# Kernel tuning notes

Measured on AMD Instinct MI355X. Metric: run time of the kernel, lower is better.

## Reference

```python
import jax, jax.numpy as jnp
import numpy as np
from jax import lax


def _conv1x1(x, w, b=None):
    # x: [B,C,H,W], w: [O,C]
    y = jnp.einsum('bchw,oc->bohw', x, w)
    if b is not None:
        y = y + b[None, :, None, None]
    return y


def _lgce(x, pre_w, pre_b, w1, b1, w2, b2, sw, sb, post_w, post_b):
    # Local Group Context Enhancer on [B,64,H,W], 8 groups of 8 channels.
    b, c, h, wd = x.shape
    g = 8
    cg = c // g
    res = x
    x = _conv1x1(x, pre_w, pre_b)
    xg = x.reshape(b, g, cg, h, wd)
    # CBAM per group (vectorized over groups)
    pooled = xg.mean(axis=(3, 4))                                  # [b,g,cg]
    hid = jax.nn.relu(jnp.einsum('bgc,ghc->bgh', pooled, w1) + b1[None])
    cw = jax.nn.sigmoid(jnp.einsum('bgh,gch->bgc', hid, w2) + b2[None])
    xc = xg * cw[:, :, :, None, None]                              # channel gate
    sp = jax.nn.sigmoid(jnp.einsum('bgchw,goc->bgohw', xc, sw) + sb[None, :, :, None, None])
    cbam_out = xc * sp                                             # spatial gate
    resp = jax.nn.sigmoid(cbam_out)
    thr = resp.mean(axis=(2, 3, 4), keepdims=True)                 # per (batch, group)
    mask = jnp.where(resp > thr, jnp.ones_like(resp), resp)
    x = (xg * mask).reshape(b, c, h, wd)
    x = _conv1x1(x, post_w, post_b)
    return x + res


def setup_inputs() -> dict:
    key = jax.random.key(0)
    ks = jax.random.split(key, 20)
    f = lambda k, s: (jax.random.normal(k, s) * 0.02).astype(jnp.float32)
    return {
        'x': jax.random.normal(ks[0], (4, 128, 256, 256), dtype=jnp.float32),
        'input_proj_w': f(ks[1], (128, 128)),
        'lgce_pre_w': f(ks[2], (64, 64)), 'lgce_pre_b': f(ks[3], (64,)),
        'cbam_w1': f(ks[4], (8, 2, 8)), 'cbam_b1': f(ks[5], (8, 2)),
        'cbam_w2': f(ks[6], (8, 8, 2)), 'cbam_b2': f(ks[7], (8, 8)),
        'cbam_sw': f(ks[8], (8, 1, 8)), 'cbam_sb': f(ks[9], (8, 1)),
        'lgce_post_w': f(ks[10], (64, 64)), 'lgce_post_b': f(ks[11], (64,)),
        'qkv_w': f(ks[12], (192, 64)),
        'dw_w': f(ks[13], (192, 1, 3, 3)),
        'gate_w1': f(ks[14], (32, 64)), 'gate_b1': f(ks[15], (32,)),
        'gate_w2': f(ks[16], (1, 32)), 'gate_b2': f(ks[17], (1,)),
        'temperature': jnp.ones((8, 1, 1), jnp.float32),
        'scales': jnp.full((4,), 0.2, jnp.float32),
        'proj_out_w': f(ks[18], (128, 128)),
    }


def reference(x, input_proj_w, lgce_pre_w, lgce_pre_b, cbam_w1, cbam_b1,
              cbam_w2, cbam_b2, cbam_sw, cbam_sb, lgce_post_w, lgce_post_b,
              qkv_w, dw_w, gate_w1, gate_b1, gate_w2, gate_b2,
              temperature, scales, proj_out_w):
    b, c, h, wd = x.shape
    heads = 8
    proj = _conv1x1(x, input_proj_w)
    lb, gb = jnp.split(proj, 2, axis=1)                            # local / global
    lb = _lgce(lb, lgce_pre_w, lgce_pre_b, cbam_w1, cbam_b1, cbam_w2, cbam_b2,
               cbam_sw, cbam_sb, lgce_post_w, lgce_post_b)
    qkv = _conv1x1(gb, qkv_w)
    qkv = lax.conv_general_dilated(qkv, dw_w, (1, 1), 'SAME',
                                   feature_group_count=192,
                                   dimension_numbers=('NCHW', 'OIHW', 'NCHW'))
    q, k, v = jnp.split(qkv, 3, axis=1)
    hw = h * wd
    cph = (c // 2) // heads                                        # channels per head
    to_heads = lambda t: t.reshape(b, heads, cph, hw)
    q, k, v = to_heads(q), to_heads(k), to_heads(v)
    q = q / jnp.maximum(jnp.linalg.norm(q, axis=-1, keepdims=True), 1e-12)
    k = k / jnp.maximum(jnp.linalg.norm(k, axis=-1, keepdims=True), 1e-12)
    attn = jnp.einsum('bhcn,bhdn->bhcd', q, k) * temperature[None]  # [b,h,cph,cph]
    # dynamic top-k from global gate (single scalar over whole batch, as original)
    gate = jax.nn.sigmoid(_conv1x1(jax.nn.relu(_conv1x1(gb, gate_w1, gate_b1)),
                                   gate_w2, gate_b2))
    kdyn = jnp.clip(jnp.floor(cph * gate.mean()), 1.0, float(cph))
    # rank-based top-k mask (jit-safe equivalent of topk+scatter)
    ranks = jnp.argsort(jnp.argsort(-attn, axis=-1), axis=-1)
    attn = jnp.where(ranks < kdyn, attn, -jnp.inf)
    attn = jax.nn.softmax(attn, axis=-1)
    out = jnp.einsum('bhcd,bhdn->bhcn', attn, v) * scales.sum()
    out = out.reshape(b, c // 2, h, wd)
    fused = jnp.concatenate([out, lb], axis=1)
    return _conv1x1(fused, proj_out_w)
```

## Files before the change

### kernel.cpp

```cpp
#include <hip/hip_runtime.h>
#include <math.h>

#define HWN 65536

__device__ __forceinline__ float sgm(float x){ return 1.0f/(1.0f+expf(-x)); }

__device__ __forceinline__ void fma4(float acc[4], const float4 w,
                                     const float4 x0, const float4 x1,
                                     const float4 x2, const float4 x3){
    acc[0] += w.x*x0.x + w.y*x1.x + w.z*x2.x + w.w*x3.x;
    acc[1] += w.x*x0.y + w.y*x1.y + w.z*x2.y + w.w*x3.y;
    acc[2] += w.x*x0.z + w.y*x1.z + w.z*x2.z + w.w*x3.z;
    acc[3] += w.x*x0.w + w.y*x1.w + w.z*x2.w + w.w*x3.w;
}

__global__ __launch_bounds__(256,2) void k1_proj(
    const float* __restrict__ x,   const float* __restrict__ Wp,
    const float* __restrict__ Wpre,const float* __restrict__ bpre,
    const float* __restrict__ Wqkv,
    const float* __restrict__ Wg1, const float* __restrict__ bg1,
    const float* __restrict__ wg2, const float* __restrict__ bg2,
    float* __restrict__ lb, float* __restrict__ pre, float* __restrict__ qkv,
    float* __restrict__ pooled_part, float* __restrict__ gate_part)
{
    __shared__ float st[128*128];
    float4* st4 = (float4*)st;
    float*  ht  = st;

    const int t    = threadIdx.x;
    const int blk  = blockIdx.x;
    const int b    = blk >> 9;
    const int p0   = (blk & 511) << 7;
    const int pg   = t & 15;
    const int og   = t >> 4;
    const int slot = blk & 63;

    const float4* x4 = (const float4*)x;

    #pragma unroll
    for (int i = 0; i < 16; ++i) {
        int idx = t + 256*i;
        int c = idx >> 5, q = idx & 31;
        st4[c*32 + q] = x4[(size_t)(b*128 + c)*16384 + (p0>>2) + q];
    }
    __syncthreads();

    {
        const int o0 = og*8;
        float acc[8][8];
        #pragma unroll
        for (int j=0;j<8;++j)
            #pragma unroll
            for (int k=0;k<8;++k) acc[j][k]=0.f;
        const float4* W4 = (const float4*)Wp;
        #pragma unroll 2
        for (int c = 0; c < 128; c += 4) {
            float4 xa0 = st4[(c+0)*32 + pg],      xb0 = st4[(c+0)*32 + 16 + pg];
            float4 xa1 = st4[(c+1)*32 + pg],      xb1 = st4[(c+1)*32 + 16 + pg];
            float4 xa2 = st4[(c+2)*32 + pg],      xb2 = st4[(c+2)*32 + 16 + pg];
            float4 xa3 = st4[(c+3)*32 + pg],      xb3 = st4[(c+3)*32 + 16 + pg];
            #pragma unroll
            for (int j = 0; j < 8; ++j) {
                float4 w = W4[(o0+j)*32 + (c>>2)];
                fma4(&acc[j][0], w, xa0,xa1,xa2,xa3);
                fma4(&acc[j][4], w, xb0,xb1,xb2,xb3);
            }
        }
        __syncthreads();

        #pragma unroll
        for (int j = 0; j < 8; ++j) {
            st4[(o0+j)*32 + pg]      = make_float4(acc[j][0],acc[j][1],acc[j][2],acc[j][3]);
            st4[(o0+j)*32 + 16 + pg] = make_float4(acc[j][4],acc[j][5],acc[j][6],acc[j][7]);
        }
        if (og < 8) {
            float4* lb4 = (float4*)lb;
            #pragma unroll
            for (int j = 0; j < 8; ++j) {
                lb4[(size_t)(b*64 + o0+j)*16384 + (p0>>2) + pg] =
                    make_float4(acc[j][0],acc[j][1],acc[j][2],acc[j][3]);
                lb4[(size_t)(b*64 + o0+j)*16384 + (p0>>2) + 16 + pg] =
                    make_float4(acc[j][4],acc[j][5],acc[j][6],acc[j][7]);
            }
        }
    }
    __syncthreads();

    {
        const int o0 = og*4;
        float acc[4][8];
        #pragma unroll
        for (int j=0;j<4;++j)
            #pragma unroll
            for (int k=0;k<8;++k) acc[j][k]=0.f;
        const float4* W4 = (const float4*)Wpre;
        #pragma unroll 2
        for (int c = 0; c < 64; c += 4) {
            float4 xa0 = st4[(c+0)*32 + pg],      xb0 = st4[(c+0)*32 + 16 + pg];
            float4 xa1 = st4[(c+1)*32 + pg],      xb1 = st4[(c+1)*32 + 16 + pg];
            float4 xa2 = st4[(c+2)*32 + pg],      xb2 = st4[(c+2)*32 + 16 + pg];
            float4 xa3 = st4[(c+3)*32 + pg],      xb3 = st4[(c+3)*32 + 16 + pg];
            #pragma unroll
            for (int j = 0; j < 4; ++j) {
                float4 w = W4[(o0+j)*16 + (c>>2)];
                fma4(&acc[j][0], w, xa0,xa1,xa2,xa3);
                fma4(&acc[j][4], w, xb0,xb1,xb2,xb3);
            }
        }
        float4* pre4 = (float4*)pre;
        #pragma unroll
        for (int j = 0; j < 4; ++j) {
            float bs = bpre[o0+j];
            float4 v0 = make_float4(acc[j][0]+bs, acc[j][1]+bs, acc[j][2]+bs, acc[j][3]+bs);
            float4 v1 = make_float4(acc[j][4]+bs, acc[j][5]+bs, acc[j][6]+bs, acc[j][7]+bs);
            pre4[(size_t)(b*64 + o0+j)*16384 + (p0>>2) + pg]      = v0;
            pre4[(size_t)(b*64 + o0+j)*16384 + (p0>>2) + 16 + pg] = v1;
            float s = v0.x+v0.y+v0.z+v0.w + v1.x+v1.y+v1.z+v1.w;
            s += __shfl_xor(s,1); s += __shfl_xor(s,2);
            s += __shfl_xor(s,4); s += __shfl_xor(s,8);
            if (pg == 0) atomicAdd(&pooled_part[slot*256 + b*64 + o0 + j], s);
        }
    }

    #pragma unroll
    for (int chk = 0; chk < 2; ++chk) {
        const int o0 = og*12 + chk*6;
        float acc[6][8];
        #pragma unroll
        for (int j=0;j<6;++j)
            #pragma unroll
            for (int k=0;k<8;++k) acc[j][k]=0.f;
        const float4* W4 = (const float4*)Wqkv;
        #pragma unroll 2
        for (int c = 0; c < 64; c += 4) {
            float4 xa0 = st4[(64+c+0)*32 + pg],   xb0 = st4[(64+c+0)*32 + 16 + pg];
            float4 xa1 = st4[(64+c+1)*32 + pg],   xb1 = st4[(64+c+1)*32 + 16 + pg];
            float4 xa2 = st4[(64+c+2)*32 + pg],   xb2 = st4[(64+c+2)*32 + 16 + pg];
            float4 xa3 = st4[(64+c+3)*32 + pg],   xb3 = st4[(64+c+3)*32 + 16 + pg];
            #pragma unroll
            for (int j = 0; j < 6; ++j) {
                float4 w = W4[(o0+j)*16 + (c>>2)];
                fma4(&acc[j][0], w, xa0,xa1,xa2,xa3);
                fma4(&acc[j][4], w, xb0,xb1,xb2,xb3);
            }
        }
        float4* qkv4 = (float4*)qkv;
        #pragma unroll
        for (int j = 0; j < 6; ++j) {
            qkv4[(size_t)(b*192 + o0+j)*16384 + (p0>>2) + pg] =
                make_float4(acc[j][0],acc[j][1],acc[j][2],acc[j][3]);
            qkv4[(size_t)(b*192 + o0+j)*16384 + (p0>>2) + 16 + pg] =
                make_float4(acc[j][4],acc[j][5],acc[j][6],acc[j][7]);
        }
    }

    {
        const int o0 = og*2;
        float acc[2][8];
        #pragma unroll
        for (int j=0;j<2;++j)
            #pragma unroll
            for (int k=0;k<8;++k) acc[j][k]=0.f;
        const float4* W4 = (const float4*)Wg1;
        for (int c = 0; c < 64; c += 4) {
            float4 xa0 = st4[(64+c+0)*32 + pg],   xb0 = st4[(64+c+0)*32 + 16 + pg];
            float4 xa1 = st4[(64+c+1)*32 + pg],   xb1 = st4[(64+c+1)*32 + 16 + pg];
            float4 xa2 = st4[(64+c+2)*32 + pg],   xb2 = st4[(64+c+2)*32 + 16 + pg];
            float4 xa3 = st4[(64+c+3)*32 + pg],   xb3 = st4[(64+c+3)*32 + 16 + pg];
            #pragma unroll
            for (int j = 0; j < 2; ++j) {
                float4 w = W4[(o0+j)*16 + (c>>2)];
                fma4(&acc[j][0], w, xa0,xa1,xa2,xa3);
                fma4(&acc[j][4], w, xb0,xb1,xb2,xb3);
            }
        }
        __syncthreads();
        #pragma unroll
        for (int j = 0; j < 2; ++j) {
            float bs = bg1[o0+j];
            #pragma unroll
            for (int k = 0; k < 4; ++k) {
                ht[(o0+j)*128 + pg*4 + k]      = fmaxf(acc[j][k]+bs,   0.0f);
                ht[(o0+j)*128 + 64 + pg*4 + k] = fmaxf(acc[j][4+k]+bs, 0.0f);
            }
        }
    }
    __syncthreads();

    if (t < 128) {
        float g = bg2[0];
        #pragma unroll
        for (int c = 0; c < 32; ++c) g += wg2[c]*ht[c*128 + t];
        g = sgm(g);
        g += __shfl_xor(g,1);  g += __shfl_xor(g,2);  g += __shfl_xor(g,4);
        g += __shfl_xor(g,8);  g += __shfl_xor(g,16); g += __shfl_xor(g,32);
        if ((t & 63) == 0) atomicAdd(&gate_part[slot], g);
    }
}

__global__ void k2_small(const float* __restrict__ pooled_part,
                         const float* __restrict__ gate_part,
                         const float* __restrict__ w1, const float* __restrict__ b1,
                         const float* __restrict__ w2, const float* __restrict__ b2,
                         float* __restrict__ cw, float* __restrict__ kdyn)
{
    __shared__ float pl[256];
    const int t = threadIdx.x;
    float s = 0.f;
    for (int sl = 0; sl < 64; ++sl) s += pooled_part[sl*256 + t];
    pl[t] = s * (1.0f/65536.0f);
    __syncthreads();
    const int b = t >> 6, g = (t >> 3) & 7, c = t & 7;
    float h0 = b1[g*2+0], h1 = b1[g*2+1];
    #pragma unroll
    for (int cc = 0; cc < 8; ++cc) {
        float p = pl[b*64 + g*8 + cc];
        h0 += p*w1[g*16 + 0*8 + cc];
        h1 += p*w1[g*16 + 1*8 + cc];
    }
    h0 = fmaxf(h0, 0.f); h1 = fmaxf(h1, 0.f);
    cw[t] = sgm(h0*w2[g*16 + c*2 + 0] + h1*w2[g*16 + c*2 + 1] + b2[g*8+c]);
    if (t == 0) {
        float gs = 0.f;
        for (int sl = 0; sl < 64; ++sl) gs += gate_part[sl];
        float kd = floorf(8.0f * (gs * (1.0f/262144.0f)));
        *kdyn = fminf(fmaxf(kd, 1.0f), 8.0f);
    }
}

#define K4_ROWSTRIDE 264
#define K4_BUF (10*K4_ROWSTRIDE)

__global__ __launch_bounds__(256,3) void k4_dw(
    const float* __restrict__ qkv, const float* __restrict__ dww,
    const float* __restrict__ pre, const float* __restrict__ cw,
    const float* __restrict__ sw,  const float* __restrict__ sb,
    float* __restrict__ v, float* __restrict__ Sg, float* __restrict__ sumsq,
    float* __restrict__ thr_sum)
{
    __shared__ float sh[2*K4_BUF];

    const int t    = threadIdx.x;
    const int b    = blockIdx.x >> 8;
    const int h    = (blockIdx.x >> 5) & 7;
    const int band = blockIdx.x & 31;
    const int r0   = band * 8;
    const int lr   = t >> 5;
    const int c0   = (t & 31) * 4;
    const int lane = t & 63;

    if (t < 40) {
        int bufi = t / 20, r = (t % 20) >> 1, side = t & 1;
        sh[bufi*K4_BUF + r*K4_ROWSTRIDE + (side ? 260 : 3)] = 0.0f;
    }

    float4 reg[3];

    auto issue_loads = [&](int ch) {
        const float4* base = (const float4*)(qkv + (size_t)(b*192 + ch)*HWN);
        #pragma unroll
        for (int j = 0; j < 3; ++j) {
            int i = t + 256*j;
            float4 val = make_float4(0.f,0.f,0.f,0.f);
            if (i < 640) {
                int row = i >> 6, col4 = i & 63;
                int gy = r0 - 1 + row;
                if (gy >= 0 && gy < 256) val = base[gy*64 + col4];
            }
            reg[j] = val;
        }
    };

    auto write_lds = [&](float* buf) {
        #pragma unroll
        for (int j = 0; j < 3; ++j) {
            int i = t + 256*j;
            if (i < 640) {
                int row = i >> 6, col4 = i & 63;
                *(float4*)&buf[row*K4_ROWSTRIDE + 4 + col4*4] = reg[j];
            }
        }
    };

    auto conv8 = [&](const float* buf, const float* __restrict__ w9, float out[8]) {
        #pragma unroll
        for (int g = 0; g < 2; ++g) {
            const int cc = c0 + g*128;
            float a0=0.f, a1=0.f, a2=0.f, a3=0.f;
            #pragma unroll
            for (int rr = 0; rr < 3; ++rr) {
                const float* row = &buf[(lr+rr)*K4_ROWSTRIDE + 4 + cc];
                float4 m = *(const float4*)row;
                float l = row[-1], r = row[4];
                float w0 = w9[rr*3+0], w1 = w9[rr*3+1], w2 = w9[rr*3+2];
                a0 = fmaf(w0,l,   fmaf(w1,m.x, fmaf(w2,m.y, a0)));
                a1 = fmaf(w0,m.x, fmaf(w1,m.y, fmaf(w2,m.z, a1)));
                a2 = fmaf(w0,m.y, fmaf(w1,m.z, fmaf(w2,m.w, a2)));
                a3 = fmaf(w0,m.z, fmaf(w1,m.w, fmaf(w2,r,   a3)));
            }
            out[g*4+0]=a0; out[g*4+1]=a1; out[g*4+2]=a2; out[g*4+3]=a3;
        }
    };

    auto wsum = [&](float val) {
        val += __shfl_xor(val,1);  val += __shfl_xor(val,2);  val += __shfl_xor(val,4);
        val += __shfl_xor(val,8);  val += __shfl_xor(val,16); val += __shfl_xor(val,32);
        return val;
    };

    float dq[8][8];

    float* sq_q = &sumsq[b*128 + h*8];
    float* sq_k = &sumsq[b*128 + 64 + h*8];
    float* Sgb  = &Sg[(size_t)(b*8+h)*64];

    issue_loads(h*8 + 0);

    #pragma unroll
    for (int ch = 0; ch < 8; ++ch) {
        float* buf = sh + (ch & 1)*K4_BUF;
        write_lds(buf);
        issue_loads(ch < 7 ? (h*8 + ch + 1) : (64 + h*8));
        __syncthreads();
        conv8(buf, dww + (h*8 + ch)*9, dq[ch]);
        float ss = 0.f;
        #pragma unroll
        for (int p = 0; p < 8; ++p) ss = fmaf(dq[ch][p], dq[ch][p], ss);
        ss = wsum(ss);
        if (lane == 0) atomicAdd(&sq_q[ch], ss);
    }

    #pragma unroll
    for (int ch = 0; ch < 8; ++ch) {
        float* buf = sh + (ch & 1)*K4_BUF;
        write_lds(buf);
        issue_loads(ch < 7 ? (64 + h*8 + ch + 1) : (128 + h*8));
        __syncthreads();
        float dk[8];
        conv8(buf, dww + (64 + h*8 + ch)*9, dk);
        float ss = 0.f;
        #pragma unroll
        for (int p = 0; p < 8; ++p) ss = fmaf(dk[p], dk[p], ss);
        ss = wsum(ss);
        if (lane == 0) atomicAdd(&sq_k[ch], ss);
        #pragma unroll
        for (int c = 0; c < 8; ++c) {
            float acc = 0.f;
            #pragma unroll
            for (int p = 0; p < 8; ++p) acc = fmaf(dq[c][p], dk[p], acc);
            acc = wsum(acc);
            if (lane == 0) atomicAdd(&Sgb[c*8 + ch], acc);
        }
    }

    #pragma unroll
    for (int ch = 0; ch < 8; ++ch) {
        float* buf = sh + (ch & 1)*K4_BUF;
        write_lds(buf);
        if (ch < 7) issue_loads(128 + h*8 + ch + 1);
        __syncthreads();
        float dv[8];
        conv8(buf, dww + (128 + h*8 + ch)*9, dv);
        float* vb = v + (size_t)(b*64 + h*8 + ch)*HWN + (r0 + lr)*256;
        *(float4*)&vb[c0]       = make_float4(dv[0],dv[1],dv[2],dv[3]);
        *(float4*)&vb[c0 + 128] = make_float4(dv[4],dv[5],dv[6],dv[7]);
    }

    {
        float cwr[8], swr[8];
        #pragma unroll
        for (int c = 0; c < 8; ++c) {
            cwr[c] = cw[b*64 + h*8 + c];
            swr[c] = sw[h*8 + c];
        }
        const float sbg = sb[h];
        float rs = 0.f;
        const float* preb = pre + (size_t)(b*64 + h*8)*HWN + (size_t)(r0 + lr)*256;
        #pragma unroll
        for (int g2 = 0; g2 < 2; ++g2) {
            const int cc = c0 + g2*128;
            float xc[8][4];
            float spa0 = sbg, spa1 = sbg, spa2 = sbg, spa3 = sbg;
            #pragma unroll
            for (int c = 0; c < 8; ++c) {
                float4 xv = *(const float4*)&preb[(size_t)c*HWN + cc];
                xc[c][0] = xv.x*cwr[c]; xc[c][1] = xv.y*cwr[c];
                xc[c][2] = xv.z*cwr[c]; xc[c][3] = xv.w*cwr[c];
                spa0 = fmaf(xc[c][0], swr[c], spa0);
                spa1 = fmaf(xc[c][1], swr[c], spa1);
                spa2 = fmaf(xc[c][2], swr[c], spa2);
                spa3 = fmaf(xc[c][3], swr[c], spa3);
            }
            float sp0 = sgm(spa0), sp1 = sgm(spa1), sp2 = sgm(spa2), sp3 = sgm(spa3);
            #pragma unroll
            for (int c = 0; c < 8; ++c) {
                rs += sgm(xc[c][0]*sp0);
                rs += sgm(xc[c][1]*sp1);
                rs += sgm(xc[c][2]*sp2);
                rs += sgm(xc[c][3]*sp3);
            }
        }
        rs = wsum(rs);
        if (lane == 0) atomicAdd(&thr_sum[b*8 + h], rs);
    }
}

__global__ void k6_attn(const float* __restrict__ Sg, const float* __restrict__ sumsq,
                        const float* __restrict__ temp, const float* __restrict__ kdynp,
                        const float* __restrict__ thr_sum, const float* __restrict__ scales,
                        float* __restrict__ A, float* __restrict__ thr)
{
    const int t = threadIdx.x;
    if (t < 32) thr[t] = thr_sum[t] * (1.0f/(8.0f*65536.0f));
    const int b = t >> 6, h = (t >> 3) & 7, c = t & 7;
    const float kd = *kdynp;
    const float ssum = scales[0]+scales[1]+scales[2]+scales[3];
    const float nq = fmaxf(sqrtf(sumsq[b*128 + h*8 + c]), 1e-12f);
    const float tv = temp[h];
    const float* Srow = Sg + (size_t)(b*8+h)*64 + c*8;
    float a[8];
    #pragma unroll
    for (int d = 0; d < 8; ++d) {
        float nk = fmaxf(sqrtf(sumsq[b*128 + 64 + h*8 + d]), 1e-12f);
        a[d] = Srow[d] / (nq*nk) * tv;
    }
    bool keep[8];
    #pragma unroll
    for (int d = 0; d < 8; ++d) {
        int r = 0;
        #pragma unroll
        for (int e = 0; e < 8; ++e)
            r += (a[e] > a[d]) || (a[e] == a[d] && e < d);
        keep[d] = ((float)r < kd);
    }
    float m = -INFINITY;
    #pragma unroll
    for (int d = 0; d < 8; ++d) if (keep[d]) m = fmaxf(m, a[d]);
    float ex[8]; float sum = 0.f;
    #pragma unroll
    for (int d = 0; d < 8; ++d) { ex[d] = keep[d] ? expf(a[d]-m) : 0.f; sum += ex[d]; }
    const float inv = ssum / sum;
    #pragma unroll
    for (int d = 0; d < 8; ++d)
        A[(size_t)(b*8+h)*64 + c*8 + d] = ex[d]*inv;
}

__global__ __launch_bounds__(256,2) void k7_final(
    const float* __restrict__ pre, const float* __restrict__ lb, const float* __restrict__ v,
    const float* __restrict__ cw,  const float* __restrict__ thr,
    const float* __restrict__ sw,  const float* __restrict__ sb,
    const float* __restrict__ A,
    const float* __restrict__ Wpost, const float* __restrict__ bpost,
    const float* __restrict__ Wout,  float* __restrict__ out)
{
    __shared__ float pr[64*128];
    __shared__ float vt[64*128];
    float4* pr4 = (float4*)pr;
    float4* vt4 = (float4*)vt;

    const int t   = threadIdx.x;
    const int blk = blockIdx.x;
    const int b   = blk >> 9;
    const int p0  = (blk & 511) << 7;
    const int pg  = t & 15;
    const int og  = t >> 4;

    const float4* pre4g = (const float4*)pre;
    const float4* v4g   = (const float4*)v;
    #pragma unroll
    for (int i = 0; i < 8; ++i) {
        int idx = t + 256*i;
        int c = idx >> 5, q = idx & 31;
        size_t gi = (size_t)(b*64 + c)*16384 + (p0>>2) + q;
        pr4[c*32+q] = pre4g[gi];
        vt4[c*32+q] = v4g[gi];
    }
    __syncthreads();

    #pragma unroll
    for (int s = 0; s < 4; ++s) {
        int task = t + 256*s;
        int g = task >> 7, px = task & 127;
        float xc[8], xv[8];
        float spa = sb[g];
        #pragma unroll
        for (int c = 0; c < 8; ++c) {
            xv[c] = pr[(g*8+c)*128 + px];
            xc[c] = xv[c]*cw[b*64 + g*8 + c];
            spa += xc[c]*sw[g*8 + c];
        }
        float sp = sgm(spa);
        float th = thr[b*8 + g];
        #pragma unroll
        for (int c = 0; c < 8; ++c) {
            float resp = sgm(xc[c]*sp);
            float mask = resp > th ? 1.0f : resp;
            pr[(g*8+c)*128 + px] = xv[c]*mask;
        }
    }
    __syncthreads();

    float postv[4][8];
    {
        const int o0 = og*4;
        float acc[4][8];
        #pragma unroll
        for (int j=0;j<4;++j)
            #pragma unroll
            for (int k=0;k<8;++k) acc[j][k]=0.f;
        const float4* W4 = (const float4*)Wpost;
        #pragma unroll 2
        for (int c = 0; c < 64; c += 4) {
            float4 xa0 = pr4[(c+0)*32 + pg],      xb0 = pr4[(c+0)*32 + 16 + pg];
            float4 xa1 = pr4[(c+1)*32 + pg],      xb1 = pr4[(c+1)*32 + 16 + pg];
            float4 xa2 = pr4[(c+2)*32 + pg],      xb2 = pr4[(c+2)*32 + 16 + pg];
            float4 xa3 = pr4[(c+3)*32 + pg],      xb3 = pr4[(c+3)*32 + 16 + pg];
            #pragma unroll
            for (int j = 0; j < 4; ++j) {
                float4 w = W4[(o0+j)*16 + (c>>2)];
                fma4(&acc[j][0], w, xa0,xa1,xa2,xa3);
                fma4(&acc[j][4], w, xb0,xb1,xb2,xb3);
            }
        }
        const float4* lb4 = (const float4*)lb;
        #pragma unroll
        for (int j = 0; j < 4; ++j) {
            float bs = bpost[o0+j];
            float4 l0 = lb4[(size_t)(b*64 + o0+j)*16384 + (p0>>2) + pg];
            float4 l1 = lb4[(size_t)(b*64 + o0+j)*16384 + (p0>>2) + 16 + pg];
            postv[j][0]=acc[j][0]+bs+l0.x; postv[j][1]=acc[j][1]+bs+l0.y;
            postv[j][2]=acc[j][2]+bs+l0.z; postv[j][3]=acc[j][3]+bs+l0.w;
            postv[j][4]=acc[j][4]+bs+l1.x; postv[j][5]=acc[j][5]+bs+l1.y;
            postv[j][6]=acc[j][6]+bs+l1.z; postv[j][7]=acc[j][7]+bs+l1.w;
        }
    }

    float attv[4][8];
    {
        const int ch0 = og*4;
        #pragma unroll
        for (int j = 0; j < 4; ++j) {
            int ch = ch0 + j;
            int hh = ch >> 3, c = ch & 7;
            const float* Ar = A + (size_t)(b*8+hh)*64 + c*8;
            float a0=0.f,a1=0.f,a2=0.f,a3=0.f,a4=0.f,a5=0.f,a6=0.f,a7=0.f;
            #pragma unroll
            for (int d = 0; d < 8; ++d) {
                float av = Ar[d];
                float4 v0 = vt4[(hh*8+d)*32 + pg];
                float4 v1 = vt4[(hh*8+d)*32 + 16 + pg];
                a0 += av*v0.x; a1 += av*v0.y; a2 += av*v0.z; a3 += av*v0.w;
                a4 += av*v1.x; a5 += av*v1.y; a6 += av*v1.z; a7 += av*v1.w;
            }
            attv[j][0]=a0; attv[j][1]=a1; attv[j][2]=a2; attv[j][3]=a3;
            attv[j][4]=a4; attv[j][5]=a5; attv[j][6]=a6; attv[j][7]=a7;
        }
    }
    __syncthreads();

    {
        const int o0 = og*4;
        #pragma unroll
        for (int j = 0; j < 4; ++j) {
            vt4[(o0+j)*32 + pg]      = make_float4(attv[j][0],attv[j][1],attv[j][2],attv[j][3]);
            vt4[(o0+j)*32 + 16 + pg] = make_float4(attv[j][4],attv[j][5],attv[j][6],attv[j][7]);
            pr4[(o0+j)*32 + pg]      = make_float4(postv[j][0],postv[j][1],postv[j][2],postv[j][3]);
            pr4[(o0+j)*32 + 16 + pg] = make_float4(postv[j][4],postv[j][5],postv[j][6],postv[j][7]);
        }
    }
    __syncthreads();

    {
        const int o0 = og*8;
        float acc[8][8];
        #pragma unroll
        for (int j=0;j<8;++j)
            #pragma unroll
            for (int k=0;k<8;++k) acc[j][k]=0.f;
        const float4* W4 = (const float4*)Wout;
        #pragma unroll 2
        for (int c = 0; c < 64; c += 4) {
            float4 xa0 = vt4[(c+0)*32 + pg],      xb0 = vt4[(c+0)*32 + 16 + pg];
            float4 xa1 = vt4[(c+1)*32 + pg],      xb1 = vt4[(c+1)*32 + 16 + pg];
            float4 xa2 = vt4[(c+2)*32 + pg],      xb2 = vt4[(c+2)*32 + 16 + pg];
            float4 xa3 = vt4[(c+3)*32 + pg],      xb3 = vt4[(c+3)*32 + 16 + pg];
            #pragma unroll
            for (int j = 0; j < 8; ++j) {
                float4 w = W4[(o0+j)*32 + (c>>2)];
                fma4(&acc[j][0], w, xa0,xa1,xa2,xa3);
                fma4(&acc[j][4], w, xb0,xb1,xb2,xb3);
            }
        }
        #pragma unroll 2
        for (int c = 0; c < 64; c += 4) {
            float4 xa0 = pr4[(c+0)*32 + pg],      xb0 = pr4[(c+0)*32 + 16 + pg];
            float4 xa1 = pr4[(c+1)*32 + pg],      xb1 = pr4[(c+1)*32 + 16 + pg];
            float4 xa2 = pr4[(c+2)*32 + pg],      xb2 = pr4[(c+2)*32 + 16 + pg];
            float4 xa3 = pr4[(c+3)*32 + pg],      xb3 = pr4[(c+3)*32 + 16 + pg];
            #pragma unroll
            for (int j = 0; j < 8; ++j) {
                float4 w = W4[(o0+j)*32 + 16 + (c>>2)];
                fma4(&acc[j][0], w, xa0,xa1,xa2,xa3);
                fma4(&acc[j][4], w, xb0,xb1,xb2,xb3);
            }
        }
        float4* out4 = (float4*)out;
        #pragma unroll
        for (int j = 0; j < 8; ++j) {
            out4[(size_t)(b*128 + o0+j)*16384 + (p0>>2) + pg] =
                make_float4(acc[j][0],acc[j][1],acc[j][2],acc[j][3]);
            out4[(size_t)(b*128 + o0+j)*16384 + (p0>>2) + 16 + pg] =
                make_float4(acc[j][4],acc[j][5],acc[j][6],acc[j][7]);
        }
    }
}

extern "C" void kernel_launch(void* const* d_in, const int* in_sizes, int n_in,
                              void* d_out, int out_size, void* d_ws, size_t ws_size,
                              hipStream_t stream)
{
    const float* x     = (const float*)d_in[0];
    const float* Wp    = (const float*)d_in[1];
    const float* Wpre  = (const float*)d_in[2];
    const float* bpre  = (const float*)d_in[3];
    const float* w1    = (const float*)d_in[4];
    const float* b1    = (const float*)d_in[5];
    const float* w2    = (const float*)d_in[6];
    const float* b2    = (const float*)d_in[7];
    const float* sw    = (const float*)d_in[8];
    const float* sb    = (const float*)d_in[9];
    const float* Wpost = (const float*)d_in[10];
    const float* bpost = (const float*)d_in[11];
    const float* Wqkv  = (const float*)d_in[12];
    const float* dww   = (const float*)d_in[13];
    const float* Wg1   = (const float*)d_in[14];
    const float* bg1   = (const float*)d_in[15];
    const float* wg2   = (const float*)d_in[16];
    const float* bg2   = (const float*)d_in[17];
    const float* temp  = (const float*)d_in[18];
    const float* scales= (const float*)d_in[19];
    const float* Wout  = (const float*)d_in[20];
    float* out = (float*)d_out;

    float* ws = (float*)d_ws;
    float* pooled_part = ws;
    float* gate_part   = ws + 16384;
    float* thr_sum     = ws + 16448;
    float* sumsq       = ws + 16480;
    float* Sg          = ws + 16992;
    float* cw          = ws + 19040;
    float* kdyn        = ws + 19296;
    float* thr         = ws + 19328;
    float* A           = ws + 19360;

    float* lb  = ws + 32768;
    float* pre = lb  + 16777216;
    float* qkv = pre + 16777216;
    float* v   = qkv + 50331648;

    hipMemsetAsync(ws, 0, (size_t)19040*sizeof(float), stream);

    k1_proj <<<2048, 256, 0, stream>>>(x, Wp, Wpre, bpre, Wqkv, Wg1, bg1, wg2, bg2,
                                       lb, pre, qkv, pooled_part, gate_part);
    k2_small<<<1,    256, 0, stream>>>(pooled_part, gate_part, w1, b1, w2, b2, cw, kdyn);
    k4_dw   <<<1024, 256, 0, stream>>>(qkv, dww, pre, cw, sw, sb, v, Sg, sumsq, thr_sum);
    k6_attn <<<1,    256, 0, stream>>>(Sg, sumsq, temp, kdyn, thr_sum, scales, A, thr);
    k7_final<<<2048, 256, 0, stream>>>(pre, lb, v, cw, thr, sw, sb, A,
                                       Wpost, bpost, Wout, out);
}
```

Baseline: 797.0 us.

## Use split-bf16 MFMA for final output projection in k7_final

Replaces the scalar FP32 FMA loop of the final 128->128 output projection with bf16 MFMA instructions. Each FP32 operand is split into hi and lo bf16 parts and three MFMAs are issued per tile to keep accuracy close to FP32. Activations are repacked into a transposed, XOR-swizzled bf16 layout in shared memory. The trade-off is extra packing work, scalar (non-vectorized) output stores, and a small precision loss from dropping the lo*lo term.

```diff
diff --git a/kernel.cpp b/kernel.cpp
--- a/kernel.cpp
+++ b/kernel.cpp
@@ -3,7 +3,14 @@
 
 #define HWN 65536
 
+typedef __attribute__((ext_vector_type(8))) short bf16x8;
+typedef __attribute__((ext_vector_type(4))) float f32x4;
+
 __device__ __forceinline__ float sgm(float x){ return 1.0f/(1.0f+expf(-x)); }
+
+__device__ __forceinline__ unsigned pack_hi2(float a, float b){
+    return (__float_as_uint(b) & 0xFFFF0000u) | (__float_as_uint(a) >> 16);
+}
 
 __device__ __forceinline__ void fma4(float acc[4], const float4 w,
                                      const float4 x0, const float4 x1,
@@ -453,10 +460,15 @@
     const float* __restrict__ Wpost, const float* __restrict__ bpost,
     const float* __restrict__ Wout,  float* __restrict__ out)
 {
-    __shared__ float pr[64*128];
-    __shared__ float vt[64*128];
+    __shared__ float smem[16384];
+    float* pr = smem;
+    float* vt = smem + 8192;
     float4* pr4 = (float4*)pr;
     float4* vt4 = (float4*)vt;
+    unsigned* XThi32 = (unsigned*)smem;
+    unsigned* XTlo32 = (unsigned*)(smem + 8192);
+    const unsigned short* XThi = (const unsigned short*)smem;
+    const unsigned short* XTlo = (const unsigned short*)(smem + 8192);
 
     const int t   = threadIdx.x;
     const int blk = blockIdx.x;
@@ -559,58 +571,79 @@
     __syncthreads();
 
     {
-        const int o0 = og*4;
-        #pragma unroll
-        for (int j = 0; j < 4; ++j) {
-            vt4[(o0+j)*32 + pg]      = make_float4(attv[j][0],attv[j][1],attv[j][2],attv[j][3]);
-            vt4[(o0+j)*32 + 16 + pg] = make_float4(attv[j][4],attv[j][5],attv[j][6],attv[j][7]);
-            pr4[(o0+j)*32 + pg]      = make_float4(postv[j][0],postv[j][1],postv[j][2],postv[j][3]);
-            pr4[(o0+j)*32 + 16 + pg] = make_float4(postv[j][4],postv[j][5],postv[j][6],postv[j][7]);
+        #pragma unroll
+        for (int half = 0; half < 2; ++half) {
+            #pragma unroll
+            for (int k = 0; k < 4; ++k) {
+                const int px = half*64 + pg*4 + k;
+                const int sw2 = (px & 7) << 2;
+                const int rowb = px*64;
+                #pragma unroll
+                for (int jj = 0; jj < 4; jj += 2) {
+                    float a0 = attv[jj][half*4+k], a1 = attv[jj+1][half*4+k];
+                    int i32 = (rowb + ((og*4+jj)>>1)) ^ sw2;
+                    XThi32[i32] = pack_hi2(a0, a1);
+                    float ah0 = __uint_as_float(__float_as_uint(a0)&0xFFFF0000u);
+                    float ah1 = __uint_as_float(__float_as_uint(a1)&0xFFFF0000u);
+                    XTlo32[i32] = pack_hi2(a0-ah0, a1-ah1);
+                    float q0 = postv[jj][half*4+k], q1 = postv[jj+1][half*4+k];
+                    i32 = (rowb + ((64+og*4+jj)>>1)) ^ sw2;
+                    XThi32[i32] = pack_hi2(q0, q1);
+                    float qh0 = __uint_as_float(__float_as_uint(q0)&0xFFFF0000u);
+                    float qh1 = __uint_as_float(__float_as_uint(q1)&0xFFFF0000u);
+                    XTlo32[i32] = pack_hi2(q0-qh0, q1-qh1);
+                }
+            }
         }
     }
     __syncthreads();
 
     {
-        const int o0 = og*8;
-        float acc[8][8];
-        #pragma unroll
-        for (int j=0;j<8;++j)
-            #pragma unroll
-            for (int k=0;k<8;++k) acc[j][k]=0.f;
-        const float4* W4 = (const float4*)Wout;
-        #pragma unroll 2
-        for (int c = 0; c < 64; c += 4) {
-            float4 xa0 = vt4[(c+0)*32 + pg],      xb0 = vt4[(c+0)*32 + 16 + pg];
-            float4 xa1 = vt4[(c+1)*32 + pg],      xb1 = vt4[(c+1)*32 + 16 + pg];
-            float4 xa2 = vt4[(c+2)*32 + pg],      xb2 = vt4[(c+2)*32 + 16 + pg];
-            float4 xa3 = vt4[(c+3)*32 + pg],      xb3 = vt4[(c+3)*32 + 16 + pg];
-            #pragma unroll
-            for (int j = 0; j < 8; ++j) {
-                float4 w = W4[(o0+j)*32 + (c>>2)];
-                fma4(&acc[j][0], w, xa0,xa1,xa2,xa3);
-                fma4(&acc[j][4], w, xb0,xb1,xb2,xb3);
-            }
-        }
-        #pragma unroll 2
-        for (int c = 0; c < 64; c += 4) {
-            float4 xa0 = pr4[(c+0)*32 + pg],      xb0 = pr4[(c+0)*32 + 16 + pg];
-            float4 xa1 = pr4[(c+1)*32 + pg],      xb1 = pr4[(c+1)*32 + 16 + pg];
-            float4 xa2 = pr4[(c+2)*32 + pg],      xb2 = pr4[(c+2)*32 + 16 + pg];
-            float4 xa3 = pr4[(c+3)*32 + pg],      xb3 = pr4[(c+3)*32 + 16 + pg];
-            #pragma unroll
-            for (int j = 0; j < 8; ++j) {
-                float4 w = W4[(o0+j)*32 + 16 + (c>>2)];
-                fma4(&acc[j][0], w, xa0,xa1,xa2,xa3);
-                fma4(&acc[j][4], w, xb0,xb1,xb2,xb3);
-            }
-        }
-        float4* out4 = (float4*)out;
-        #pragma unroll
-        for (int j = 0; j < 8; ++j) {
-            out4[(size_t)(b*128 + o0+j)*16384 + (p0>>2) + pg] =
-                make_float4(acc[j][0],acc[j][1],acc[j][2],acc[j][3]);
-            out4[(size_t)(b*128 + o0+j)*16384 + (p0>>2) + 16 + pg] =
-                make_float4(acc[j][4],acc[j][5],acc[j][6],acc[j][7]);
+        const int lane = t & 63, wv = t >> 6;
+        const int lm = lane & 15, lq = lane >> 4;
+        #pragma unroll
+        for (int oo = 0; oo < 2; ++oo) {
+            const int ot = wv*2 + oo;
+            f32x4 acc[8];
+            #pragma unroll
+            for (int pt = 0; pt < 8; ++pt) { acc[pt][0]=0.f; acc[pt][1]=0.f; acc[pt][2]=0.f; acc[pt][3]=0.f; }
+            const int orow = ot*16 + lm;
+            #pragma unroll
+            for (int kk = 0; kk < 4; ++kk) {
+                const int cbase = kk*32 + lq*8;
+                const float* wp = Wout + orow*128 + cbase;
+                float4 w0 = *(const float4*)wp;
+                float4 w1 = *(const float4*)(wp+4);
+                float we[8] = {w0.x,w0.y,w0.z,w0.w,w1.x,w1.y,w1.z,w1.w};
+                bf16x8 Ahi, Alo;
+                #pragma unroll
+                for (int d = 0; d < 4; ++d) {
+                    float e0 = we[2*d], e1 = we[2*d+1];
+                    ((unsigned*)&Ahi)[d] = pack_hi2(e0, e1);
+                    float h0 = __uint_as_float(__float_as_uint(e0)&0xFFFF0000u);
+                    float h1 = __uint_as_float(__float_as_uint(e1)&0xFFFF0000u);
+                    ((unsigned*)&Alo)[d] = pack_hi2(e0-h0, e1-h1);
+                }
+                #pragma unroll
+                for (int pt = 0; pt < 8; ++pt) {
+                    const int px = pt*16 + lm;
+                    const int idx = (px*128 + cbase) ^ ((px&7)<<3);
+                    bf16x8 Bhi = *(const bf16x8*)&XThi[idx];
+                    bf16x8 Blo = *(const bf16x8*)&XTlo[idx];
+                    acc[pt] = __builtin_amdgcn_mfma_f32_16x16x32_bf16(Ahi, Bhi, acc[pt], 0,0,0);
+                    acc[pt] = __builtin_amdgcn_mfma_f32_16x16x32_bf16(Ahi, Blo, acc[pt], 0,0,0);
+                    acc[pt] = __builtin_amdgcn_mfma_f32_16x16x32_bf16(Alo, Bhi, acc[pt], 0,0,0);
+                }
+            }
+            #pragma unroll
+            for (int pt = 0; pt < 8; ++pt) {
+                const int px = p0 + pt*16 + lm;
+                #pragma unroll
+                for (int r = 0; r < 4; ++r) {
+                    const int ch = ot*16 + lq*4 + r;
+                    out[(size_t)(b*128 + ch)*HWN + px] = acc[pt][r];
+                }
+            }
         }
     }
 }
```

New measurement: 736.8 us. -7.5%, faster.
